# Kernel tuning notes

Measured on AMD Instinct MI355X. Metric: run time of the kernel, lower is better.

## Reference

```python
import jax, jax.numpy as jnp
import numpy as np

KSIZE = 13
DIL = 3
NUM_HEADS = 4
LN_EPS = 1e-5


def _na_idx(L, k, d):
    # NATTEN-style dilated neighborhood indices along one axis.
    i = jnp.arange(L)
    g, ii = i % d, i // d                       # dilation group, index within group
    Lg = (L - g + d - 1) // d                   # group length per position
    start = jnp.clip(ii - k // 2, 0, Lg - k)    # clamped window start (group coords)
    offs = jnp.arange(k)
    nbr = g[:, None] + d * (start[:, None] + offs[None, :])           # (L,k) absolute idx
    rel = start[:, None] + offs[None, :] - ii[:, None] + (k - 1)      # (L,k) rpb index in [0,2k-2]
    return nbr, rel


def _layernorm(x, g, b):
    mu = jnp.mean(x, -1, keepdims=True)
    var = jnp.mean(jnp.square(x - mu), -1, keepdims=True)
    return (x - mu) * jax.lax.rsqrt(var + LN_EPS) * g + b


def setup_inputs() -> dict:
    key = jax.random.key(0)
    ks = jax.random.split(key, 12)
    B, H, W, C = 1, 96, 96, 64
    mh = int(C * 4.0)
    s = 0.02
    return {
        "x": jax.random.normal(ks[0], (B, H * W, C), jnp.float32),
        "norm1_g": jnp.ones((C,), jnp.float32),
        "norm1_b": jnp.zeros((C,), jnp.float32),
        "qkv_w": jax.random.normal(ks[1], (C, 3 * C), jnp.float32) * s,
        "qkv_b": jnp.zeros((3 * C,), jnp.float32),
        "rpb": jax.random.normal(ks[2], (NUM_HEADS, 2 * KSIZE - 1, 2 * KSIZE - 1), jnp.float32) * s,
        "proj_w": jax.random.normal(ks[3], (C, C), jnp.float32) * s,
        "proj_b": jnp.zeros((C,), jnp.float32),
        "norm2_g": jnp.ones((C,), jnp.float32),
        "norm2_b": jnp.zeros((C,), jnp.float32),
        "fc1_w": jax.random.normal(ks[4], (C, mh), jnp.float32) * s,
        "fc1_b": jnp.zeros((mh,), jnp.float32),
        "fc2_w": jax.random.normal(ks[5], (mh, C), jnp.float32) * s,
        "fc2_b": jnp.zeros((C,), jnp.float32),
        "H": H,
        "W": W,
    }


def _ga(h, qkv_w, qkv_b, rpb, proj_w, proj_b):
    # h: (B,H,W,C) -> dilated neighborhood attention, kernel=13, dilation=3
    B, H, W, C = h.shape
    nh, hd = NUM_HEADS, C // NUM_HEADS
    scale = hd ** -0.5
    qkv = (h @ qkv_w + qkv_b).reshape(B, H, W, 3, nh, hd)
    qkv = qkv.transpose(3, 0, 4, 1, 2, 5)       # (3,B,nh,H,W,hd)
    q, k, v = qkv[0] * scale, qkv[1], qkv[2]
    idx_h, rel_h = _na_idx(H, KSIZE, DIL)
    idx_w, rel_w = _na_idx(W, KSIZE, DIL)
    Kk = KSIZE

    def gather(t):  # (B,nh,H,W,hd) -> (B,nh,H,W,Kk*Kk,hd)
        t = jnp.take(t, idx_h, axis=2)          # (B,nh,H,Kk,W,hd)
        t = jnp.take(t, idx_w, axis=4)          # (B,nh,H,Kk,W,Kk,hd)
        return t.transpose(0, 1, 2, 4, 3, 5, 6).reshape(B, nh, H, W, Kk * Kk, hd)

    kg = gather(k)
    vg = gather(v)
    logits = jnp.einsum('bnhwc,bnhwkc->bnhwk', q, kg)
    bias = rpb[:, rel_h]                         # (nh,H,Kk,2K-1)
    bias = bias[:, :, :, rel_w]                  # (nh,H,Kk,W,Kk)
    bias = bias.transpose(0, 1, 3, 2, 4).reshape(nh, H, W, Kk * Kk)
    attn = jax.nn.softmax(logits + bias[None], axis=-1)
    out = jnp.einsum('bnhwk,bnhwkc->bnhwc', attn, vg)
    out = out.transpose(0, 2, 3, 1, 4).reshape(B, H, W, C)
    return out @ proj_w + proj_b


def reference(x, norm1_g, norm1_b, qkv_w, qkv_b, rpb, proj_w, proj_b,
              norm2_g, norm2_b, fc1_w, fc1_b, fc2_w, fc2_b, H, W):
    B, N, C = x.shape
    shortcut = x
    h = _layernorm(x, norm1_g, norm1_b).reshape(B, H, W, C)
    h = _ga(h, qkv_w, qkv_b, rpb, proj_w, proj_b).reshape(B, N, C)
    x = shortcut + h
    h2 = _layernorm(x, norm2_g, norm2_b)
    mlp = jax.nn.gelu(h2 @ fc1_w + fc1_b, approximate=False) @ fc2_w + fc2_b
    return x + mlp
```

## Files before the change

kernel.cpp:

```cpp
#include <hip/hip_runtime.h>
#include <math.h>

#define HH 96
#define WW 96
#define CC 64
#define NH 4
#define HD 16
#define KS 13
#define KK (KS*KS)
#define NTOK (HH*WW)

__device__ __forceinline__ float dpp_reduce8(float p) {
    int t;
    t = __builtin_amdgcn_update_dpp(0, __float_as_int(p), 0xB1, 0xF, 0xF, true);
    p += __int_as_float(t);
    t = __builtin_amdgcn_update_dpp(0, __float_as_int(p), 0x4E, 0xF, 0xF, true);
    p += __int_as_float(t);
    t = __builtin_amdgcn_update_dpp(0, __float_as_int(p), 0x141, 0xF, 0xF, true);
    p += __int_as_float(t);
    return p;
}
__device__ __forceinline__ float dpp_reduce16(float p) {
    p = dpp_reduce8(p);
    int t = __builtin_amdgcn_update_dpp(0, __float_as_int(p), 0x140, 0xF, 0xF, true);
    p += __int_as_float(t);
    return p;
}

__device__ __forceinline__ void ln_rows32(float (*buf)[34],
                                          const float* __restrict__ g,
                                          const float* __restrict__ b,
                                          int tid) {
    int r  = tid >> 3;
    int c0 = (tid & 7) * 8;
    float v[8];
    float s = 0.0f;
    #pragma unroll
    for (int j = 0; j < 8; j++) { v[j] = buf[c0 + j][r]; s += v[j]; }
    s = dpp_reduce8(s);
    float mu = s * (1.0f / 64.0f);
    float s2 = 0.0f;
    #pragma unroll
    for (int j = 0; j < 8; j++) { float d = v[j] - mu; s2 += d * d; }
    s2 = dpp_reduce8(s2);
    float inv = rsqrtf(s2 * (1.0f / 64.0f) + 1e-5f);
    #pragma unroll
    for (int j = 0; j < 8; j++)
        buf[c0 + j][r] = (v[j] - mu) * inv * g[c0 + j] + b[c0 + j];
}

__global__ __launch_bounds__(256) void ln_gemm_kernel(const float* __restrict__ x,
                                                      const float* __restrict__ g,
                                                      const float* __restrict__ b,
                                                      const float* __restrict__ W,
                                                      const float* __restrict__ bias,
                                                      float* __restrict__ out) {
    __shared__ float Ast[64][34];
    const int t0 = blockIdx.x * 32;
    const int tid = threadIdx.x;

    for (int i = tid; i < 32 * 64; i += 256) {
        int r = i >> 6, cc = i & 63;
        Ast[cc][r] = x[t0 * 64 + i];
    }
    __syncthreads();
    ln_rows32(Ast, g, b, tid);
    __syncthreads();

    const int tc = tid & 15;
    const int tr = tid >> 4;
    const int r0 = tr * 2;
    const int c  = blockIdx.y * 64 + tc * 4;

    float4 b4 = *(const float4*)&bias[c];
    float4 acc0 = b4, acc1 = b4;
    #pragma unroll 8
    for (int k = 0; k < 64; k++) {
        float2 a = *(const float2*)&Ast[k][r0];
        float4 w = *(const float4*)&W[k * 192 + c];
        acc0.x += a.x * w.x; acc0.y += a.x * w.y; acc0.z += a.x * w.z; acc0.w += a.x * w.w;
        acc1.x += a.y * w.x; acc1.y += a.y * w.y; acc1.z += a.y * w.z; acc1.w += a.y * w.w;
    }
    if (blockIdx.y == 0) {
        acc0.x *= 0.25f; acc0.y *= 0.25f; acc0.z *= 0.25f; acc0.w *= 0.25f;
        acc1.x *= 0.25f; acc1.y *= 0.25f; acc1.z *= 0.25f; acc1.w *= 0.25f;
    }
    *(float4*)&out[(t0 + r0) * 192 + c] = acc0;
    *(float4*)&out[(t0 + r0 + 1) * 192 + c] = acc1;
}

__global__ __launch_bounds__(256) void na_attn_kernel(const float* __restrict__ qkv,
                                                      const float* __restrict__ rpb,
                                                      float* __restrict__ out) {
    int wave = threadIdx.x >> 6;
    int lane = threadIdx.x & 63;
    int token = blockIdx.x * 4 + wave;
    int head = lane >> 4;
    int dim  = lane & 15;

    int y = token / WW, x = token - y * WW;
    int gh = y % 3, ih = y / 3;
    int gw = x % 3, iw = x / 3;
    int sh = ih - 6; sh = sh < 0 ? 0 : (sh > 19 ? 19 : sh);
    int sw = iw - 6; sw = sw < 0 ? 0 : (sw > 19 ? 19 : sw);

    int co = head * HD + dim;
    float q = qkv[token * 192 + co];
    const float* bias_h = rpb + head * 625 + (sw - iw + 12);

    float acc = 0.0f, s = 0.0f;
    for (int kh = 0; kh < KS; kh++) {
        int ny = gh + 3 * (sh + kh);
        int rh = sh + kh - ih + 12;
        const float* kp = qkv + (ny * WW + gw + 3 * sw) * 192 + 64 + co;
        const float* bp = bias_h + rh * 25;
        #pragma unroll
        for (int kw = 0; kw < KS; kw++) {
            float kv = kp[kw * 576];
            float vv = kp[kw * 576 + 64];
            float p = dpp_reduce16(q * kv);
            float e = __expf(p + bp[kw]);
            s += e;
            acc += e * vv;
        }
    }
    out[token * CC + co] = acc / s;
}

__global__ __launch_bounds__(256) void mlp_fused_kernel(const float* __restrict__ attn_out,
                                                        const float* __restrict__ x,
                                                        const float* __restrict__ proj_w,
                                                        const float* __restrict__ proj_b,
                                                        const float* __restrict__ n2g,
                                                        const float* __restrict__ n2b,
                                                        const float* __restrict__ fc1_w,
                                                        const float* __restrict__ fc1_b,
                                                        const float* __restrict__ fc2_w,
                                                        const float* __restrict__ fc2_b,
                                                        float* __restrict__ out) {
    __shared__ float Ast[64][34];
    __shared__ float X2T[64][34];
    __shared__ float Hid[256][34];

    const int t0 = blockIdx.x * 32;
    const int tid = threadIdx.x;

    for (int i = tid; i < 32 * 64; i += 256) {
        int r = i >> 6, cc = i & 63;
        Ast[cc][r] = attn_out[t0 * 64 + i];
    }
    __syncthreads();

    const int tc = tid & 15;
    const int tr = tid >> 4;
    const int r0 = tr * 2;
    const int c  = tc * 4;

    float4 pb = *(const float4*)&proj_b[c];
    float4 a0 = pb, a1 = pb;
    #pragma unroll 8
    for (int k = 0; k < 64; k++) {
        float2 a = *(const float2*)&Ast[k][r0];
        float4 w = *(const float4*)&proj_w[k * 64 + c];
        a0.x += a.x * w.x; a0.y += a.x * w.y; a0.z += a.x * w.z; a0.w += a.x * w.w;
        a1.x += a.y * w.x; a1.y += a.y * w.y; a1.z += a.y * w.z; a1.w += a.y * w.w;
    }
    {
        float4 x0 = *(const float4*)&x[(t0 + r0) * 64 + c];
        float4 x1 = *(const float4*)&x[(t0 + r0 + 1) * 64 + c];
        a0.x += x0.x; a0.y += x0.y; a0.z += x0.z; a0.w += x0.w;
        a1.x += x1.x; a1.y += x1.y; a1.z += x1.z; a1.w += x1.w;
    }
    X2T[c + 0][r0] = a0.x; X2T[c + 1][r0] = a0.y; X2T[c + 2][r0] = a0.z; X2T[c + 3][r0] = a0.w;
    X2T[c + 0][r0 + 1] = a1.x; X2T[c + 1][r0 + 1] = a1.y; X2T[c + 2][r0 + 1] = a1.z; X2T[c + 3][r0 + 1] = a1.w;
    __syncthreads();

    ln_rows32(X2T, n2g, n2b, tid);
    __syncthreads();

    float4 h0[4], h1[4];
    #pragma unroll
    for (int gg = 0; gg < 4; gg++) {
        float4 bb = *(const float4*)&fc1_b[c + gg * 64];
        h0[gg] = bb; h1[gg] = bb;
    }
    #pragma unroll 4
    for (int k = 0; k < 64; k++) {
        float2 a = *(const float2*)&X2T[k][r0];
        #pragma unroll
        for (int gg = 0; gg < 4; gg++) {
            float4 w = *(const float4*)&fc1_w[k * 256 + c + gg * 64];
            h0[gg].x += a.x * w.x; h0[gg].y += a.x * w.y; h0[gg].z += a.x * w.z; h0[gg].w += a.x * w.w;
            h1[gg].x += a.y * w.x; h1[gg].y += a.y * w.y; h1[gg].z += a.y * w.z; h1[gg].w += a.y * w.w;
        }
    }
    #define GELU1(v) v = 0.5f * v * (1.0f + erff(v * 0.70710678118f))
    #pragma unroll
    for (int gg = 0; gg < 4; gg++) {
        GELU1(h0[gg].x); GELU1(h0[gg].y); GELU1(h0[gg].z); GELU1(h0[gg].w);
        GELU1(h1[gg].x); GELU1(h1[gg].y); GELU1(h1[gg].z); GELU1(h1[gg].w);
    }
    #undef GELU1
    #pragma unroll
    for (int gg = 0; gg < 4; gg++) {
        int col = c + gg * 64;
        Hid[col + 0][r0] = h0[gg].x; Hid[col + 1][r0] = h0[gg].y;
        Hid[col + 2][r0] = h0[gg].z; Hid[col + 3][r0] = h0[gg].w;
        Hid[col + 0][r0 + 1] = h1[gg].x; Hid[col + 1][r0 + 1] = h1[gg].y;
        Hid[col + 2][r0 + 1] = h1[gg].z; Hid[col + 3][r0 + 1] = h1[gg].w;
    }
    __syncthreads();

    float4 ob = *(const float4*)&fc2_b[c];
    float4 o0 = ob, o1 = ob;
    #pragma unroll 8
    for (int k = 0; k < 256; k++) {
        float2 a = *(const float2*)&Hid[k][r0];
        float4 w = *(const float4*)&fc2_w[k * 64 + c];
        o0.x += a.x * w.x; o0.y += a.x * w.y; o0.z += a.x * w.z; o0.w += a.x * w.w;
        o1.x += a.y * w.x; o1.y += a.y * w.y; o1.z += a.y * w.z; o1.w += a.y * w.w;
    }
    o0.x += a0.x; o0.y += a0.y; o0.z += a0.z; o0.w += a0.w;
    o1.x += a1.x; o1.y += a1.y; o1.z += a1.z; o1.w += a1.w;
    *(float4*)&out[(t0 + r0) * 64 + c] = o0;
    *(float4*)&out[(t0 + r0 + 1) * 64 + c] = o1;
}

extern "C" void kernel_launch(void* const* d_in, const int* in_sizes, int n_in,
                              void* d_out, int out_size, void* d_ws, size_t ws_size,
                              hipStream_t stream) {
    const float* x       = (const float*)d_in[0];
    const float* norm1_g = (const float*)d_in[1];
    const float* norm1_b = (const float*)d_in[2];
    const float* qkv_w   = (const float*)d_in[3];
    const float* qkv_b   = (const float*)d_in[4];
    const float* rpb     = (const float*)d_in[5];
    const float* proj_w  = (const float*)d_in[6];
    const float* proj_b  = (const float*)d_in[7];
    const float* norm2_g = (const float*)d_in[8];
    const float* norm2_b = (const float*)d_in[9];
    const float* fc1_w   = (const float*)d_in[10];
    const float* fc1_b   = (const float*)d_in[11];
    const float* fc2_w   = (const float*)d_in[12];
    const float* fc2_b   = (const float*)d_in[13];
    float* out = (float*)d_out;

    float* ws = (float*)d_ws;
    float* qkv      = ws;
    float* attn_out = qkv + NTOK * 192;

    dim3 blk(256);
    ln_gemm_kernel<<<dim3(NTOK / 32, 3), blk, 0, stream>>>(x, norm1_g, norm1_b, qkv_w, qkv_b, qkv);
    na_attn_kernel<<<NTOK / 4, blk, 0, stream>>>(qkv, rpb, attn_out);
    mlp_fused_kernel<<<NTOK / 32, blk, 0, stream>>>(attn_out, x, proj_w, proj_b,
                                                    norm2_g, norm2_b, fc1_w, fc1_b,
                                                    fc2_w, fc2_b, out);
}
```

Before: 177.6 us.

## Split attention neighbors across lane slots with float4 head-dim vectors

The neighborhood attention kernel is remapped so each lane holds four head dimensions as float4, and four lane slots per head work on different kw neighbors in parallel. This cuts the per-neighbor DPP reduction from four steps to two and the inner loop from 13 iterations to about 4. Partial softmax sums and accumulators are combined across slots at the end with row-rotate DPP adds. The cost is an uneven tail, since slot 0 handles the 13th column alone, plus an extra final cross-slot reduction.

```diff
diff --git a/kernel.cpp b/kernel.cpp
--- a/kernel.cpp
+++ b/kernel.cpp
@@ -10,20 +10,16 @@
 #define KK (KS*KS)
 #define NTOK (HH*WW)
 
+template<int CTRL>
+__device__ __forceinline__ float dpp_add(float p) {
+    int t = __builtin_amdgcn_update_dpp(0, __float_as_int(p), CTRL, 0xF, 0xF, true);
+    return p + __int_as_float(t);
+}
+
 __device__ __forceinline__ float dpp_reduce8(float p) {
-    int t;
-    t = __builtin_amdgcn_update_dpp(0, __float_as_int(p), 0xB1, 0xF, 0xF, true);
-    p += __int_as_float(t);
-    t = __builtin_amdgcn_update_dpp(0, __float_as_int(p), 0x4E, 0xF, 0xF, true);
-    p += __int_as_float(t);
-    t = __builtin_amdgcn_update_dpp(0, __float_as_int(p), 0x141, 0xF, 0xF, true);
-    p += __int_as_float(t);
-    return p;
-}
-__device__ __forceinline__ float dpp_reduce16(float p) {
-    p = dpp_reduce8(p);
-    int t = __builtin_amdgcn_update_dpp(0, __float_as_int(p), 0x140, 0xF, 0xF, true);
-    p += __int_as_float(t);
+    p = dpp_add<0xB1>(p);
+    p = dpp_add<0x4E>(p);
+    p = dpp_add<0x141>(p);
     return p;
 }
 
@@ -96,7 +92,9 @@
     int lane = threadIdx.x & 63;
     int token = blockIdx.x * 4 + wave;
     int head = lane >> 4;
-    int dim  = lane & 15;
+    int slot = (lane >> 2) & 3;
+    int l    = lane & 3;
+    int co   = head * HD + l * 4;
 
     int y = token / WW, x = token - y * WW;
     int gh = y % 3, ih = y / 3;
@@ -104,27 +102,52 @@
     int sh = ih - 6; sh = sh < 0 ? 0 : (sh > 19 ? 19 : sh);
     int sw = iw - 6; sw = sw < 0 ? 0 : (sw > 19 ? 19 : sw);
 
-    int co = head * HD + dim;
-    float q = qkv[token * 192 + co];
+    float4 q4 = *(const float4*)&qkv[token * 192 + co];
     const float* bias_h = rpb + head * 625 + (sw - iw + 12);
 
-    float acc = 0.0f, s = 0.0f;
+    const int xpart = (gw + 3 * sw) * 192 + 64 + co + slot * 576;
+
+    float4 acc = make_float4(0.f, 0.f, 0.f, 0.f);
+    float s = 0.0f;
+
     for (int kh = 0; kh < KS; kh++) {
         int ny = gh + 3 * (sh + kh);
-        int rh = sh + kh - ih + 12;
-        const float* kp = qkv + (ny * WW + gw + 3 * sw) * 192 + 64 + co;
-        const float* bp = bias_h + rh * 25;
+        const float* kp = qkv + ny * (WW * 192) + xpart;
+        const float* bp = bias_h + (sh + kh - ih + 12) * 25;
         #pragma unroll
-        for (int kw = 0; kw < KS; kw++) {
-            float kv = kp[kw * 576];
-            float vv = kp[kw * 576 + 64];
-            float p = dpp_reduce16(q * kv);
-            float e = __expf(p + bp[kw]);
+        for (int i = 0; i < 3; i++) {
+            float4 k4 = *(const float4*)(kp + i * 2304);
+            float4 v4 = *(const float4*)(kp + i * 2304 + 64);
+            float p = q4.x * k4.x + q4.y * k4.y + q4.z * k4.z + q4.w * k4.w;
+            p = dpp_add<0xB1>(p);
+            p = dpp_add<0x4E>(p);
+            float e = __expf(p + bp[4 * i + slot]);
             s += e;
-            acc += e * vv;
+            acc.x += e * v4.x; acc.y += e * v4.y; acc.z += e * v4.z; acc.w += e * v4.w;
         }
-    }
-    out[token * CC + co] = acc / s;
+        if (slot == 0) {
+            float4 k4 = *(const float4*)(kp + 3 * 2304);
+            float4 v4 = *(const float4*)(kp + 3 * 2304 + 64);
+            float p = q4.x * k4.x + q4.y * k4.y + q4.z * k4.z + q4.w * k4.w;
+            p = dpp_add<0xB1>(p);
+            p = dpp_add<0x4E>(p);
+            float e = __expf(p + bp[12]);
+            s += e;
+            acc.x += e * v4.x; acc.y += e * v4.y; acc.z += e * v4.z; acc.w += e * v4.w;
+        }
+    }
+
+    s = dpp_add<0x128>(s);  s = dpp_add<0x124>(s);
+    acc.x = dpp_add<0x128>(acc.x); acc.x = dpp_add<0x124>(acc.x);
+    acc.y = dpp_add<0x128>(acc.y); acc.y = dpp_add<0x124>(acc.y);
+    acc.z = dpp_add<0x128>(acc.z); acc.z = dpp_add<0x124>(acc.z);
+    acc.w = dpp_add<0x128>(acc.w); acc.w = dpp_add<0x124>(acc.w);
+
+    if (slot == 0) {
+        float inv = 1.0f / s;
+        *(float4*)&out[token * CC + co] =
+            make_float4(acc.x * inv, acc.y * inv, acc.z * inv, acc.w * inv);
+    }
 }
 
 __global__ __launch_bounds__(256) void mlp_fused_kernel(const float* __restrict__ attn_out,
```

Result: faster. 171.7 us (-3.3%).
